# Optimization experiments

Measured on AMD Instinct MI355X. Metric: run time of the kernel, lower is better.

The kernel has to match this reference:

```python
import jax, jax.numpy as jnp
import numpy as np

T, B, CIN, V = 4, 16, 2, 128
E, H, DEPTH, NC = 512, 8, 6, 11
HID = 4 * E
TAU = 2.0
EPS = 1e-5
ALPHA = 4.0  # sigmoid surrogate width (spikingjelly default)


@jax.custom_vjp
def spike(x):
    return (x >= 0.0).astype(x.dtype)

def _spike_fwd(x):
    return spike(x), x

def _spike_bwd(x, g):
    s = jax.nn.sigmoid(ALPHA * x)
    return (g * ALPHA * s * (1.0 - s),)

spike.defvjp(_spike_fwd, _spike_bwd)


def lif(x, vth):
    # x: [T, ...]; LIF with decay_input=True, v_reset=0 (hard reset)
    def step(v, xt):
        v = v + (xt - v) / TAU
        s = spike(v - vth)
        return v * (1.0 - s), s
    return jax.lax.scan(step, jnp.zeros_like(x[0]), x)[1]


def bn(x, p):
    # x: [T,B,C,V], p: [4,C] = (gamma, beta, mean, var); inference-mode BN
    g, b, m, v = p
    inv = g / jnp.sqrt(v + EPS)
    return (x - m[:, None]) * inv[:, None] + b[:, None]


def conv1x1(x, w):
    # kernel-size-1 Conv1d == channel matmul
    return jnp.einsum('tbcv,oc->tbov', x, w)


def attention(x, w, bnp):
    # w: [4,C,C] (q,k,v,proj); bnp: [4,2,4,C] (RepConv bn + extra bn)
    t, b_, C, v_ = x.shape
    c = C // H
    h = lif(x, 1.0)

    def branch(i):
        return bn(bn(conv1x1(h, w[i]), bnp[i, 0]), bnp[i, 1])

    def heads(z):  # [T,B,C,V] -> [T,B,H,N,c], channel split heads-major
        return z.reshape(t, b_, H, c, v_).transpose(0, 1, 2, 4, 3)

    q = heads(lif(branch(0), 1.0))
    k = heads(lif(branch(1), 1.0))
    vv = heads(lif(branch(2), 1.0))
    kv = jnp.einsum('tbhnc,tbhnd->tbhcd', k, vv)      # linear attention: k^T v
    o = jnp.einsum('tbhnc,tbhcd->tbhnd', q, kv) * 0.125
    o = o.transpose(0, 1, 2, 4, 3).reshape(t, b_, C, v_)
    a = lif(o, 0.5)
    return bn(bn(conv1x1(a, w[3]), bnp[3, 0]), bnp[3, 1])


def mlp(x, w1, b1, p1, w2, b2, p2):
    h = lif(x, 1.0)
    h = bn(conv1x1(h, w1) + b1[:, None], p1)
    h = lif(h, 1.0)
    return bn(conv1x1(h, w2) + b2[:, None], p2)


def _mk_bn(key, lead, c):
    k1, k2, k3, k4 = jax.random.split(key, 4)
    g = 1.0 + 0.1 * jax.random.normal(k1, (*lead, c))
    b = 0.1 * jax.random.normal(k2, (*lead, c))
    m = 0.1 * jax.random.normal(k3, (*lead, c))
    v = jax.random.uniform(k4, (*lead, c), minval=0.5, maxval=1.5)
    return jnp.stack([g, b, m, v], axis=-2)


def setup_inputs() -> dict:
    key = jax.random.key(0)
    ks = jax.random.split(key, 16)
    std = 0.02
    return {
        'x': jax.random.normal(ks[0], (T, B, CIN, V), dtype=jnp.float32),
        'pe_w': std * jax.random.normal(ks[1], (E, CIN)),
        'pe_bn': _mk_bn(ks[2], (), E),
        'qkvp_w': std * jax.random.normal(ks[3], (DEPTH, 4, E, E)),
        'qkvp_bn': _mk_bn(ks[4], (DEPTH, 4, 2), E),
        'fc1_w': std * jax.random.normal(ks[5], (DEPTH, HID, E)),
        'fc1_b': jnp.zeros((DEPTH, HID)),
        'fc1_bn': _mk_bn(ks[6], (DEPTH,), HID),
        'fc2_w': std * jax.random.normal(ks[7], (DEPTH, E, HID)),
        'fc2_b': jnp.zeros((DEPTH, E)),
        'fc2_bn': _mk_bn(ks[8], (DEPTH,), E),
        'head_w': std * jax.random.normal(ks[9], (NC, E)),
        'head_b': jnp.zeros((NC,)),
    }


def reference(x, pe_w, pe_bn, qkvp_w, qkvp_bn, fc1_w, fc1_b, fc1_bn,
              fc2_w, fc2_b, fc2_bn, head_w, head_b):
    # patch embed (first layer: no LIF)
    h = bn(conv1x1(x, pe_w), pe_bn)
    for d in range(DEPTH):
        h = h + attention(h, qkvp_w[d], qkvp_bn[d])
        h = h + mlp(h, fc1_w[d], fc1_b[d], fc1_bn[d], fc2_w[d], fc2_b[d], fc2_bn[d])
    h = h.mean(axis=3)          # [T,B,E]
    s = lif(h, 1.0)             # head_lif
    out = (s @ head_w.T + head_b).mean(axis=0)  # [B,NC]
    return out
```

## Files before the change

### kernel.cpp

```cpp
#include <hip/hip_runtime.h>

#define TT 4
#define BB 16
#define VV 128
#define EE 512
#define HIDC 2048
#define BN_EPS 1e-5f

typedef unsigned int u32;
typedef unsigned long long u64;
typedef unsigned short u16;
typedef unsigned char u8;


__global__ __launch_bounds__(256) void trans_all(const float* __restrict__ qw,
    const float* __restrict__ f1w, const float* __restrict__ f2w,
    float* __restrict__ wq, float* __restrict__ w1, float* __restrict__ w2)
{
  const int d = blockIdx.z, zz = blockIdx.y;
  const float* src; float* dst; int O, C;
  if (zz < 4)      { src = qw + ((size_t)d * 4 + zz) * EE * EE; dst = wq + ((size_t)d * 4 + zz) * EE * EE; O = EE; C = EE; }
  else if (zz == 4){ src = f1w + (size_t)d * HIDC * EE; dst = w1 + (size_t)d * HIDC * EE; O = HIDC; C = EE; }
  else             { src = f2w + (size_t)d * EE * HIDC; dst = w2 + (size_t)d * EE * HIDC; O = EE; C = HIDC; }
  const int tc_n = C >> 5, to_n = O >> 5;
  const int bx = blockIdx.x;
  if (bx >= tc_n * to_n) return;
  const int tc = bx % tc_n, to = bx / tc_n;
  __shared__ float t[32][33];
  const int tx = threadIdx.x & 31, ty = threadIdx.x >> 5;
#pragma unroll
  for (int k = 0; k < 4; ++k) {
    int o = to * 32 + ty + k * 8, c = tc * 32 + tx;
    t[ty + k * 8][tx] = src[(size_t)o * C + c];
  }
  __syncthreads();
#pragma unroll
  for (int k = 0; k < 4; ++k) {
    int c = tc * 32 + ty + k * 8, o = to * 32 + tx;
    dst[(size_t)c * O + o] = t[tx][ty + k * 8];
  }
}

__global__ __launch_bounds__(256) void pe_lif(const float* __restrict__ x,
    const float* __restrict__ w, const float* __restrict__ bnp,
    float* __restrict__ h, u32* __restrict__ mIn,
    u32* __restrict__ cnt, u16* __restrict__ ids)
{
  const int b = blockIdx.x, eb = blockIdx.y;
  const int tid = threadIdx.x;
  const int chl = tid >> 4, e = eb * 16 + chl;
  const int vs = (tid & 15) * 8;
  __shared__ u8 sB[16][16];
  __shared__ u8 sActAny[16];
  if (tid < 16) sActAny[tid] = 0;
  const float w0 = w[e * 2], w1 = w[e * 2 + 1];
  const float gg = bnp[e], be = bnp[EE + e], mm = bnp[2 * EE + e], vr = bnp[3 * EE + e];
  const float sc = gg / sqrtf(vr + BN_EPS);
  float vm[8];
#pragma unroll
  for (int k = 0; k < 8; ++k) vm[k] = 0.f;
  __syncthreads();
  for (int t = 0; t < TT; ++t) {
    const int tb = t * BB + b;
    const float* xb = x + (size_t)tb * 2 * VV + vs;
    float4 x0a = *(const float4*)&xb[0],   x0b = *(const float4*)&xb[4];
    float4 x1a = *(const float4*)&xb[VV],  x1b = *(const float4*)&xb[VV + 4];
    float a[8] = {x0a.x, x0a.y, x0a.z, x0a.w, x0b.x, x0b.y, x0b.z, x0b.w};
    float c1[8] = {x1a.x, x1a.y, x1a.z, x1a.w, x1b.x, x1b.y, x1b.z, x1b.w};
    u32 byte = 0;
#pragma unroll
    for (int k = 0; k < 8; ++k) {
      a[k] = (w0 * a[k] + w1 * c1[k] - mm) * sc + be;
      vm[k] += (a[k] - vm[k]) * 0.5f;
      float sp = (vm[k] >= 1.f) ? 1.f : 0.f;
      vm[k] *= (1.f - sp);
      byte |= (sp != 0.f) ? (1u << k) : 0u;
    }
    size_t ho = ((size_t)tb * EE + e) * VV + vs;
    float4 ha = {a[0], a[1], a[2], a[3]}, hb = {a[4], a[5], a[6], a[7]};
    *(float4*)&h[ho] = ha; *(float4*)&h[ho + 4] = hb;
    sB[chl][tid & 15] = (u8)byte;
    __syncthreads();
    if (tid < 16) {
      uint4 mw = *(const uint4*)&sB[tid][0];
      *(uint4*)&mIn[((size_t)b * EE + eb * 16 + tid) * 16 + t * 4] = mw;
      if (mw.x | mw.y | mw.z | mw.w) sActAny[tid] = 1;
    }
    __syncthreads();
  }
  if (tid == 0) {
    int c = 0;
    for (int i = 0; i < 16; ++i)
      if (sActAny[i]) ids[((size_t)b * 32 + eb) * 16 + c++] = (u16)(eb * 16 + i);
    cnt[(size_t)b * 32 + eb] = c;
  }
}

__global__ __launch_bounds__(256) void gemm_fused(
    const u32* __restrict__ InM, const u32* __restrict__ cntI,
    const u16* __restrict__ idsI, int nblkI,
    const float* __restrict__ WT, float* __restrict__ OutPre,
    const float* __restrict__ resid, u32* __restrict__ SpkM,
    u32* __restrict__ cntO, u16* __restrict__ idsO,
    const float* __restrict__ bias, const float* __restrict__ bn1,
    const float* __restrict__ bn2,
    int C, int O, float vth, long wtZ, long spkZ, long bnZ)
{
  const int b = blockIdx.x, ob = blockIdx.y * 16, z = blockIdx.z;
  const int tid = threadIdx.x, lane = tid & 63, wv = tid >> 6;
  WT += (long)z * wtZ; SpkM += (long)z * spkZ;
  if (bn1) bn1 += (long)z * bnZ;
  if (bn2) bn2 += (long)z * bnZ;

  __shared__ u16 slist[2048];
  __shared__ alignas(16) float sW[64][16];
  __shared__ alignas(16) u32 sM[64][16];
  __shared__ u32 sWS[2];
  __shared__ u32 runbS;
  __shared__ u8 sAct[16];

  const int og = (tid >> 5) * 2;
  const int vg = tid & 31;
  const int wword = vg >> 3;
  const int sh4 = (vg & 7) * 4;
  const bool hasb = (bias != nullptr), has1 = (bn1 != nullptr), has2 = (bn2 != nullptr);

  float bs[2], m1c[2], s1c[2], b1c[2], m2c[2], s2c[2], b2c[2];
#pragma unroll
  for (int k = 0; k < 2; ++k) {
    int o = ob + og + k;
    bs[k] = hasb ? bias[o] : 0.f;
    if (has1) { float g = bn1[o]; b1c[k] = bn1[O + o]; m1c[k] = bn1[2 * O + o];
                s1c[k] = g / sqrtf(bn1[3 * O + o] + BN_EPS); }
    if (has2) { float g = bn2[o]; b2c[k] = bn2[O + o]; m2c[k] = bn2[2 * O + o];
                s2c[k] = g / sqrtf(bn2[3 * O + o] + BN_EPS); }
  }

  u32 c = 0;
  if (tid < nblkI) c = cntI[(size_t)b * nblkI + tid];
  u32 xs = c;
#pragma unroll
  for (int off = 1; off < 64; off <<= 1) {
    u32 y = __shfl_up(xs, off);
    if (lane >= off) xs += y;
  }
  if (lane == 63 && wv < 2) sWS[wv] = xs;
  __syncthreads();
  if (tid < nblkI && c) {
    u32 o = ((wv == 1) ? sWS[0] : 0u) + xs - c;
    const u16* src = idsI + ((size_t)b * nblkI + tid) * 16;
    for (u32 k = 0; k < c; ++k) slist[o + k] = src[k];
  }
  if (tid == 0) runbS = sWS[0] + ((nblkI > 64) ? sWS[1] : 0u);
  __syncthreads();
  const int n = (int)runbS;

  const u32* Mb = InM + (size_t)b * C * 16;
  const float* WTb = WT + ob;

  float acc[TT][2][4] = {};
  for (int a0 = 0; a0 < n; a0 += 64) {
    int m = n - a0; if (m > 64) m = 64;
    if (a0) __syncthreads();
    {
      int cc = tid >> 2, part = tid & 3;
      if (cc < m) {
        int ch = slist[a0 + cc];
        *(float4*)&sW[cc][part * 4] = *(const float4*)&WTb[(size_t)ch * O + part * 4];
        *(uint4*)&sM[cc][part * 4]  = *(const uint4*)&Mb[(size_t)ch * 16 + part * 4];
      }
    }
    __syncthreads();
#pragma unroll 2
    for (int i = 0; i < m; ++i) {
      float2 w2 = *(const float2*)&sW[i][og];
#pragma unroll
      for (int t = 0; t < TT; ++t) {
        u32 wd = sM[i][t * 4 + wword];
        if (wd) {
          u32 nib = wd >> sh4;
          float f0 = (float)(nib & 1u);
          float f1 = (float)((nib >> 1) & 1u);
          float f2 = (float)((nib >> 2) & 1u);
          float f3 = (float)((nib >> 3) & 1u);
          acc[t][0][0] += w2.x * f0; acc[t][0][1] += w2.x * f1;
          acc[t][0][2] += w2.x * f2; acc[t][0][3] += w2.x * f3;
          acc[t][1][0] += w2.y * f0; acc[t][1][1] += w2.y * f1;
          acc[t][1][2] += w2.y * f2; acc[t][1][3] += w2.y * f3;
        }
      }
    }
  }

  float st[2][4] = {};
  u32 actU[2] = {0, 0};
#pragma unroll
  for (int t = 0; t < TT; ++t) {
    const int tb = t * BB + b;
#pragma unroll
    for (int k = 0; k < 2; ++k) {
      float a[4] = {acc[t][k][0], acc[t][k][1], acc[t][k][2], acc[t][k][3]};
      if (hasb) {
#pragma unroll
        for (int j = 0; j < 4; ++j) a[j] += bs[k];
      }
      if (has1) {
#pragma unroll
        for (int j = 0; j < 4; ++j) a[j] = (a[j] - m1c[k]) * s1c[k] + b1c[k];
      }
      if (has2) {
#pragma unroll
        for (int j = 0; j < 4; ++j) a[j] = (a[j] - m2c[k]) * s2c[k] + b2c[k];
      }
      if (OutPre) {
        size_t oi = ((size_t)tb * O + ob + og + k) * VV + vg * 4;
        float4 r = *(const float4*)&resid[oi];
        a[0] += r.x; a[1] += r.y; a[2] += r.z; a[3] += r.w;
        float4 wr = {a[0], a[1], a[2], a[3]};
        *(float4*)&OutPre[oi] = wr;
      }
      u32 nib = 0;
#pragma unroll
      for (int j = 0; j < 4; ++j) {
        st[k][j] += (a[j] - st[k][j]) * 0.5f;
        float sp = (st[k][j] >= vth) ? 1.f : 0.f;
        st[k][j] *= (1.f - sp);
        nib |= (sp != 0.f) ? (1u << j) : 0u;
      }
      u32 wmask = nib << sh4;
      wmask |= __shfl_xor(wmask, 1);
      wmask |= __shfl_xor(wmask, 2);
      wmask |= __shfl_xor(wmask, 4);
      if ((vg & 7) == 0)
        SpkM[((size_t)b * O + ob + og + k) * 16 + t * 4 + wword] = wmask;
      u32 aw = wmask | __shfl_xor(wmask, 8);
      aw |= __shfl_xor(aw, 16);
      actU[k] |= aw;
    }
  }
  if (vg == 0) { sAct[og] = actU[0] ? 1 : 0; sAct[og + 1] = actU[1] ? 1 : 0; }
  if (cntO) {
    __syncthreads();
    if (tid == 0) {
      int cc = 0;
      for (int i = 0; i < 16; ++i)
        if (sAct[i])
          idsO[((size_t)b * gridDim.y + blockIdx.y) * 16 + cc++] = (u16)(ob + i);
      cntO[(size_t)b * gridDim.y + blockIdx.y] = cc;
    }
  }
}

__global__ __launch_bounds__(256) void attn_fused(const u32* __restrict__ Qm,
    const u32* __restrict__ Km, const u32* __restrict__ Vm, u32* __restrict__ Om,
    u32* __restrict__ cntO, u16* __restrict__ idsO)
{
  const int b = blockIdx.x, hh = blockIdx.y, dq = blockIdx.z;
  const int tid = threadIdx.x, lane = tid & 63, wave = tid >> 6;
  __shared__ u64 sKm[TT][64][2];
  __shared__ u64 sVm[TT][16][2];
  __shared__ alignas(16) u32 sQw[TT][64][4];
  __shared__ u8 sQnz[TT][64];
  __shared__ alignas(16) float sKV[64][20];
  __shared__ u8 sAct[16];

  {
    int c = tid >> 2, t = tid & 3;
    size_t rb = ((size_t)b * EE + hh * 64 + c) * 16 + t * 4;
    uint4 q = *(const uint4*)&Qm[rb];
    *(uint4*)&sQw[t][c][0] = q;
    sQnz[t][c] = (q.x | q.y | q.z | q.w) ? 1 : 0;
    uint4 k = *(const uint4*)&Km[rb];
    sKm[t][c][0] = ((u64)k.y << 32) | k.x;
    sKm[t][c][1] = ((u64)k.w << 32) | k.z;
    if (c < 16) {
      uint4 v = *(const uint4*)&Vm[((size_t)b * EE + hh * 64 + dq * 16 + c) * 16 + t * 4];
      sVm[t][c][0] = ((u64)v.y << 32) | v.x;
      sVm[t][c][1] = ((u64)v.w << 32) | v.z;
    }
  }
  __syncthreads();

  const int np = lane * 2;
  const int qword = lane >> 4, qsh = np & 31;
  float acc[TT][4][2] = {};
  for (int t = 0; t < TT; ++t) {
    {
      int c = tid >> 2, d0 = (tid & 3) * 4;
      u64 k0 = sKm[t][c][0], k1 = sKm[t][c][1];
#pragma unroll
      for (int i = 0; i < 4; ++i) {
        int d = d0 + i;
        sKV[c][d] = (float)(__popcll(k0 & sVm[t][d][0]) + __popcll(k1 & sVm[t][d][1]));
      }
    }
    __syncthreads();
    for (int c = 0; c < 64; ++c) {
      if (!sQnz[t][c]) continue;
      u32 two = (sQw[t][c][qword] >> qsh) & 3u;
      if (two) {
        float f0 = (float)(two & 1u);
        float f1 = (float)(two >> 1);
        float4 kv = *(const float4*)&sKV[c][wave * 4];
        acc[t][0][0] += kv.x * f0; acc[t][0][1] += kv.x * f1;
        acc[t][1][0] += kv.y * f0; acc[t][1][1] += kv.y * f1;
        acc[t][2][0] += kv.z * f0; acc[t][2][1] += kv.z * f1;
        acc[t][3][0] += kv.w * f0; acc[t][3][1] += kv.w * f1;
      }
    }
    __syncthreads();
  }

  float st[4][2] = {};
  u32 actU[4] = {0, 0, 0, 0};
#pragma unroll
  for (int t = 0; t < TT; ++t) {
#pragma unroll
    for (int i = 0; i < 4; ++i) {
      float a0 = acc[t][i][0] * 0.125f, a1 = acc[t][i][1] * 0.125f;
      st[i][0] += (a0 - st[i][0]) * 0.5f;
      st[i][1] += (a1 - st[i][1]) * 0.5f;
      float s0 = (st[i][0] >= 0.5f) ? 1.f : 0.f;
      float s1 = (st[i][1] >= 0.5f) ? 1.f : 0.f;
      st[i][0] *= (1.f - s0); st[i][1] *= (1.f - s1);
      u32 two = ((s0 != 0.f) ? 1u : 0u) | ((s1 != 0.f) ? 2u : 0u);
      u32 wmask = two << qsh;
      wmask |= __shfl_xor(wmask, 1);
      wmask |= __shfl_xor(wmask, 2);
      wmask |= __shfl_xor(wmask, 4);
      wmask |= __shfl_xor(wmask, 8);
      if ((lane & 15) == 0)
        Om[((size_t)b * EE + hh * 64 + dq * 16 + wave * 4 + i) * 16 + t * 4 + qword] = wmask;
      u32 aw = wmask | __shfl_xor(wmask, 16);
      aw |= __shfl_xor(aw, 32);
      actU[i] |= aw;
    }
  }
  if (lane == 0) {
#pragma unroll
    for (int i = 0; i < 4; ++i) sAct[wave * 4 + i] = actU[i] ? 1 : 0;
  }
  __syncthreads();
  if (tid == 0) {
    int slot = hh * 4 + dq;
    int c = 0;
    for (int i = 0; i < 16; ++i)
      if (sAct[i]) idsO[((size_t)b * 32 + slot) * 16 + c++] = (u16)(hh * 64 + dq * 16 + i);
    cntO[(size_t)b * 32 + slot] = c;
  }
}

__global__ __launch_bounds__(256) void mean_lif(const float* __restrict__ h,
    float* __restrict__ sh)
{
  int i = blockIdx.x * 256 + threadIdx.x;
  float v = 0.f;
#pragma unroll
  for (int t = 0; t < TT; ++t) {
    const float* p = h + ((size_t)t * BB * EE + i) * VV;
    float s = 0.f;
#pragma unroll
    for (int q = 0; q < VV; q += 4) {
      float4 x = *(const float4*)&p[q];
      s += x.x + x.y + x.z + x.w;
    }
    float hm = s * (1.f / 128.f);
    v += (hm - v) * 0.5f;
    float sp = (v >= 1.f) ? 1.f : 0.f;
    sh[(size_t)t * (BB * EE) + i] = sp;
    v *= (1.f - sp);
  }
}

__global__ __launch_bounds__(256) void head_k2(const float* __restrict__ sh,
    const float* __restrict__ hw, const float* __restrict__ hb,
    float* __restrict__ out)
{
  int g = blockIdx.x * 4 + (threadIdx.x >> 6);
  int lane = threadIdx.x & 63;
  if (g >= BB * 11) return;
  int b = g / 11, n = g % 11;
  float s = 0.f;
#pragma unroll
  for (int t = 0; t < TT; ++t) {
    const float* sp = sh + (size_t)t * (BB * EE) + b * EE;
    const float* wp = hw + n * EE;
    float ss = 0.f;
#pragma unroll
    for (int e = 0; e < EE; e += 64) ss += sp[e + lane] * wp[e + lane];
#pragma unroll
    for (int off = 32; off; off >>= 1) ss += __shfl_down(ss, off);
    if (lane == 0) s += ss;
  }
  if (lane == 0) out[g] = s * 0.25f + hb[n];
}

extern "C" void kernel_launch(void* const* d_in, const int* in_sizes, int n_in,
                              void* d_out, int out_size, void* d_ws, size_t ws_size,
                              hipStream_t stream) {
  const float* x       = (const float*)d_in[0];
  const float* pe_w    = (const float*)d_in[1];
  const float* pe_bn   = (const float*)d_in[2];
  const float* qkvp_w  = (const float*)d_in[3];
  const float* qkvp_bn = (const float*)d_in[4];
  const float* fc1_w   = (const float*)d_in[5];
  const float* fc1_b   = (const float*)d_in[6];
  const float* fc1_bn  = (const float*)d_in[7];
  const float* fc2_w   = (const float*)d_in[8];
  const float* fc2_b   = (const float*)d_in[9];
  const float* fc2_bn  = (const float*)d_in[10];
  const float* head_w  = (const float*)d_in[11];
  const float* head_b  = (const float*)d_in[12];
  float* out = (float*)d_out;

  const size_t NH = (size_t)TT * BB * EE * VV;
  float* ws = (float*)d_ws;
  float* h   = ws;
  float* wq  = h + NH;
  float* w1  = wq + (size_t)6 * 4 * EE * EE;
  float* w2  = w1 + (size_t)6 * HIDC * EE;
  float* sh  = w2 + (size_t)6 * EE * HIDC;
  u32* mIn  = (u32*)(sh + (size_t)TT * BB * EE);
  u32* mQKV = mIn + (size_t)BB * EE * 16;
  u32* mO   = mQKV + (size_t)3 * BB * EE * 16;
  u32* mMlp = mO + (size_t)BB * EE * 16;
  u32* mHid = mMlp + (size_t)BB * EE * 16;
  u32* cntIn = mHid + (size_t)BB * HIDC * 16;
  u32* cntO  = cntIn + BB * 32;
  u32* cntM  = cntO + BB * 32;
  u32* cntH  = cntM + BB * 32;
  u16* idsIn = (u16*)(cntH + BB * 128);
  u16* idsO  = idsIn + (size_t)BB * 32 * 16;
  u16* idsM  = idsO + (size_t)BB * 32 * 16;
  u16* idsH  = idsM + (size_t)BB * 32 * 16;

  u32* mQ = mQKV;
  u32* mK = mQKV + (size_t)BB * EE * 16;
  u32* mV = mQKV + (size_t)2 * BB * EE * 16;

  trans_all<<<dim3(1024, 6, 6), 256, 0, stream>>>(qkvp_w, fc1_w, fc2_w, wq, w1, w2);
  pe_lif<<<dim3(BB, EE / 16), 256, 0, stream>>>(x, pe_w, pe_bn, h, mIn, cntIn, idsIn);

  for (int d = 0; d < 6; ++d) {
    const float* bn1p = qkvp_bn + (size_t)d * 4 * 2 * 4 * EE;
    gemm_fused<<<dim3(BB, EE / 16, 3), 256, 0, stream>>>(mIn, cntIn, idsIn, 32,
        wq + (size_t)d * 4 * EE * EE, nullptr, nullptr, mQ, nullptr, nullptr,
        nullptr, bn1p, bn1p + 4 * EE, EE, EE, 1.f,
        (long)EE * EE, (long)BB * EE * 16, (long)2 * 4 * EE);
    attn_fused<<<dim3(BB, 8, 4), 256, 0, stream>>>(mQ, mK, mV, mO, cntO, idsO);
    gemm_fused<<<dim3(BB, EE / 16, 1), 256, 0, stream>>>(mO, cntO, idsO, 32,
        wq + ((size_t)d * 4 + 3) * EE * EE, h, h, mMlp, cntM, idsM,
        nullptr, bn1p + 3 * (2 * 4 * EE), bn1p + 3 * (2 * 4 * EE) + 4 * EE,
        EE, EE, 1.f, 0, 0, 0);
    gemm_fused<<<dim3(BB, HIDC / 16, 1), 256, 0, stream>>>(mMlp, cntM, idsM, 32,
        w1 + (size_t)d * HIDC * EE, nullptr, nullptr, mHid, cntH, idsH,
        fc1_b + (size_t)d * HIDC, fc1_bn + (size_t)d * 4 * HIDC, nullptr,
        EE, HIDC, 1.f, 0, 0, 0);
    gemm_fused<<<dim3(BB, EE / 16, 1), 256, 0, stream>>>(mHid, cntH, idsH, 128,
        w2 + (size_t)d * EE * HIDC, h, h, mIn, cntIn, idsIn,
        fc2_b + (size_t)d * EE, fc2_bn + (size_t)d * 4 * EE, nullptr,
        HIDC, EE, 1.f, 0, 0, 0);
  }

  mean_lif<<<32, 256, 0, stream>>>(h, sh);
  head_k2<<<44, 256, 0, stream>>>(sh, head_w, head_b, out);
}
```

Before: 516.8 us.

## Transpose spike bitmask layout to word-major and batch attention KV over timesteps

Changes the per-channel spike bitmask layout from [t][word] to [word][t], so the GEMM inner loop loads all four timesteps' words for a lane with one 16-byte shared load. Producers (embed, gemm, attention) write the new layout and attention reads it with scalar loads. Attention now computes the K^T V popcount tile for all timesteps at once into a larger shared buffer, which removes the per-timestep barriers. In exchange it uses more shared memory and does more strided, narrower global stores and loads in the producer and consumer code.

```diff
diff --git a/kernel.cpp b/kernel.cpp
--- a/kernel.cpp
+++ b/kernel.cpp
@@ -83,7 +83,11 @@
     __syncthreads();
     if (tid < 16) {
       uint4 mw = *(const uint4*)&sB[tid][0];
-      *(uint4*)&mIn[((size_t)b * EE + eb * 16 + tid) * 16 + t * 4] = mw;
+      size_t base = ((size_t)b * EE + eb * 16 + tid) * 16;
+      mIn[base + 0 * 4 + t] = mw.x;
+      mIn[base + 1 * 4 + t] = mw.y;
+      mIn[base + 2 * 4 + t] = mw.z;
+      mIn[base + 3 * 4 + t] = mw.w;
       if (mw.x | mw.y | mw.z | mw.w) sActAny[tid] = 1;
     }
     __syncthreads();
@@ -174,9 +178,11 @@
 #pragma unroll 2
     for (int i = 0; i < m; ++i) {
       float2 w2 = *(const float2*)&sW[i][og];
+      uint4 m4 = *(const uint4*)&sM[i][wword * 4];
+      u32 wds[4] = {m4.x, m4.y, m4.z, m4.w};
 #pragma unroll
       for (int t = 0; t < TT; ++t) {
-        u32 wd = sM[i][t * 4 + wword];
+        u32 wd = wds[t];
         if (wd) {
           u32 nib = wd >> sh4;
           float f0 = (float)(nib & 1u);
@@ -232,7 +238,7 @@
       wmask |= __shfl_xor(wmask, 2);
       wmask |= __shfl_xor(wmask, 4);
       if ((vg & 7) == 0)
-        SpkM[((size_t)b * O + ob + og + k) * 16 + t * 4 + wword] = wmask;
+        SpkM[((size_t)b * O + ob + og + k) * 16 + wword * 4 + t] = wmask;
       u32 aw = wmask | __shfl_xor(wmask, 8);
       aw |= __shfl_xor(aw, 16);
       actU[k] |= aw;
@@ -259,56 +265,54 @@
   const int tid = threadIdx.x, lane = tid & 63, wave = tid >> 6;
   __shared__ u64 sKm[TT][64][2];
   __shared__ u64 sVm[TT][16][2];
-  __shared__ alignas(16) u32 sQw[TT][64][4];
+  __shared__ u32 sQw[TT][64][4];
   __shared__ u8 sQnz[TT][64];
-  __shared__ alignas(16) float sKV[64][20];
+  __shared__ alignas(16) float sKV[TT][64][20];
   __shared__ u8 sAct[16];
 
   {
     int c = tid >> 2, t = tid & 3;
-    size_t rb = ((size_t)b * EE + hh * 64 + c) * 16 + t * 4;
-    uint4 q = *(const uint4*)&Qm[rb];
-    *(uint4*)&sQw[t][c][0] = q;
-    sQnz[t][c] = (q.x | q.y | q.z | q.w) ? 1 : 0;
-    uint4 k = *(const uint4*)&Km[rb];
-    sKm[t][c][0] = ((u64)k.y << 32) | k.x;
-    sKm[t][c][1] = ((u64)k.w << 32) | k.z;
+    size_t rb = ((size_t)b * EE + hh * 64 + c) * 16 + t;
+    u32 q0 = Qm[rb], q1 = Qm[rb + 4], q2 = Qm[rb + 8], q3 = Qm[rb + 12];
+    sQw[t][c][0] = q0; sQw[t][c][1] = q1; sQw[t][c][2] = q2; sQw[t][c][3] = q3;
+    sQnz[t][c] = (q0 | q1 | q2 | q3) ? 1 : 0;
+    u32 k0 = Km[rb], k1 = Km[rb + 4], k2 = Km[rb + 8], k3 = Km[rb + 12];
+    sKm[t][c][0] = ((u64)k1 << 32) | k0;
+    sKm[t][c][1] = ((u64)k3 << 32) | k2;
     if (c < 16) {
-      uint4 v = *(const uint4*)&Vm[((size_t)b * EE + hh * 64 + dq * 16 + c) * 16 + t * 4];
-      sVm[t][c][0] = ((u64)v.y << 32) | v.x;
-      sVm[t][c][1] = ((u64)v.w << 32) | v.z;
-    }
-  }
-  __syncthreads();
-
-  const int np = lane * 2;
-  const int qword = lane >> 4, qsh = np & 31;
+      size_t rv = ((size_t)b * EE + hh * 64 + dq * 16 + c) * 16 + t;
+      u32 v0 = Vm[rv], v1 = Vm[rv + 4], v2 = Vm[rv + 8], v3 = Vm[rv + 12];
+      sVm[t][c][0] = ((u64)v1 << 32) | v0;
+      sVm[t][c][1] = ((u64)v3 << 32) | v2;
+    }
+  }
+  __syncthreads();
+  {
+    int c = tid >> 2, t = tid & 3;
+    u64 k0 = sKm[t][c][0], k1 = sKm[t][c][1];
+#pragma unroll
+    for (int d = 0; d < 16; ++d)
+      sKV[t][c][d] = (float)(__popcll(k0 & sVm[t][d][0]) + __popcll(k1 & sVm[t][d][1]));
+  }
+  __syncthreads();
+
+  const int qword = lane >> 4, qsh = (lane & 15) * 2;
   float acc[TT][4][2] = {};
-  for (int t = 0; t < TT; ++t) {
-    {
-      int c = tid >> 2, d0 = (tid & 3) * 4;
-      u64 k0 = sKm[t][c][0], k1 = sKm[t][c][1];
-#pragma unroll
-      for (int i = 0; i < 4; ++i) {
-        int d = d0 + i;
-        sKV[c][d] = (float)(__popcll(k0 & sVm[t][d][0]) + __popcll(k1 & sVm[t][d][1]));
-      }
-    }
-    __syncthreads();
+#pragma unroll
+  for (int t = 0; t < TT; ++t) {
     for (int c = 0; c < 64; ++c) {
       if (!sQnz[t][c]) continue;
       u32 two = (sQw[t][c][qword] >> qsh) & 3u;
       if (two) {
         float f0 = (float)(two & 1u);
         float f1 = (float)(two >> 1);
-        float4 kv = *(const float4*)&sKV[c][wave * 4];
+        float4 kv = *(const float4*)&sKV[t][c][wave * 4];
         acc[t][0][0] += kv.x * f0; acc[t][0][1] += kv.x * f1;
         acc[t][1][0] += kv.y * f0; acc[t][1][1] += kv.y * f1;
         acc[t][2][0] += kv.z * f0; acc[t][2][1] += kv.z * f1;
         acc[t][3][0] += kv.w * f0; acc[t][3][1] += kv.w * f1;
       }
     }
-    __syncthreads();
   }
 
   float st[4][2] = {};
@@ -330,7 +334,7 @@
       wmask |= __shfl_xor(wmask, 4);
       wmask |= __shfl_xor(wmask, 8);
       if ((lane & 15) == 0)
-        Om[((size_t)b * EE + hh * 64 + dq * 16 + wave * 4 + i) * 16 + t * 4 + qword] = wmask;
+        Om[((size_t)b * EE + hh * 64 + dq * 16 + wave * 4 + i) * 16 + qword * 4 + t] = wmask;
       u32 aw = wmask | __shfl_xor(wmask, 16);
       aw |= __shfl_xor(aw, 32);
       actU[i] |= aw;
```

Measured after the change: 505.1 us. 1.02x faster.
